# Kernel tuning notes

Measured on AMD Instinct MI355X. Metric: run time of the kernel, lower is better.

Reference implementation:

```python
import jax, jax.numpy as jnp
import numpy as np

TOKENS, IN_DIM, HID, OUT_DIM = 32768, 256, 1024, 256
N_EXP, TOP_K = 8, 2


def setup_inputs() -> dict:
    key = jax.random.key(0)
    ks = jax.random.split(key, 6)
    s_in = 1.0 / np.sqrt(IN_DIM)
    s_hid = 1.0 / np.sqrt(HID)
    return {
        "x": jax.random.normal(ks[0], (TOKENS, IN_DIM), dtype=jnp.float32),
        "Wg": jax.random.uniform(ks[1], (IN_DIM, N_EXP), jnp.float32, -s_in, s_in),
        "W1": jax.random.uniform(ks[2], (N_EXP, IN_DIM, HID), jnp.float32, -s_in, s_in),
        "b1": jax.random.uniform(ks[3], (N_EXP, HID), jnp.float32, -s_in, s_in),
        "W2": jax.random.uniform(ks[4], (N_EXP, HID, OUT_DIM), jnp.float32, -s_hid, s_hid),
        "b2": jax.random.uniform(ks[5], (N_EXP, OUT_DIM), jnp.float32, -s_hid, s_hid),
    }


def reference(x, Wg, W1, b1, W2, b2):
    # Router: softmax over expert logits, pick top-k, renormalize weights
    logits = x @ Wg                                  # [B, E]
    router_probs = jax.nn.softmax(logits, axis=-1)   # [B, E]
    top_w, top_idx = jax.lax.top_k(router_probs, TOP_K)  # [B, K]
    top_w = top_w / jnp.sum(top_w, axis=-1, keepdims=True)
    # Dense all-expert compute (faithful to the torch.stack over experts)
    h = jax.nn.relu(jnp.einsum("bi,eih->beh", x, W1) + b1[None])   # [B, E, H]
    expert_out = jnp.einsum("beh,eho->beo", h, W2) + b2[None]       # [B, E, O]
    # Gather top-k experts per token and combine
    selected = jnp.take_along_axis(expert_out, top_idx[:, :, None], axis=1)  # [B, K, O]
    output = jnp.sum(selected * top_w[:, :, None], axis=1)                   # [B, O]
    return output, router_probs
```

## Files before the change

kernel.cpp:

```cpp
#include <hip/hip_runtime.h>
#include <hip/hip_bf16.h>
#include <stdint.h>

#define T_TOK 32768
#define IN_D  256
#define HID_D 1024
#define OUT_D 256
#define NE    8
#define BM    64
#define HC    32
#define NCH   (HID_D / HC)

typedef unsigned short u16;
typedef __attribute__((ext_vector_type(8))) __bf16 bf16x8;
typedef __attribute__((ext_vector_type(4))) float f32x4;
typedef __attribute__((ext_vector_type(4))) unsigned int u32x4;
typedef __attribute__((ext_vector_type(2))) unsigned int u32x2;

__device__ __forceinline__ u16 f2bf(float f) {
  unsigned int u = __builtin_bit_cast(unsigned int, f);
  u = (u + 0x7FFFu + ((u >> 16) & 1u)) >> 16;
  return (u16)u;
}

__device__ __forceinline__ void gload_lds16(const u16* g, u16* l) {
  __builtin_amdgcn_global_load_lds(
      (const __attribute__((address_space(1))) unsigned int*)g,
      (__attribute__((address_space(3))) unsigned int*)l, 16, 0, 0);
}

__global__ __launch_bounds__(64) void pack_w1_kernel(const float* __restrict__ W1,
                                                     u16* __restrict__ w1p) {
  int b = blockIdx.x;
  int f = b & 15, c = (b >> 4) & 31, e = b >> 9;
  int l = threadIdx.x, l15 = l & 15, l4 = l >> 4;
  int h = c * 32 + (f >> 3) * 16 + l15;
  int k0 = (f & 7) * 32 + l4 * 8;
  unsigned int w[4];
#pragma unroll
  for (int p = 0; p < 4; ++p) {
    u16 a = f2bf(W1[((size_t)e * IN_D + k0 + 2 * p) * HID_D + h]);
    u16 bq = f2bf(W1[((size_t)e * IN_D + k0 + 2 * p + 1) * HID_D + h]);
    w[p] = (unsigned int)a | ((unsigned int)bq << 16);
  }
  *reinterpret_cast<u32x4*>(w1p + (size_t)b * 512 + l * 8) = u32x4{w[0], w[1], w[2], w[3]};
}

__global__ __launch_bounds__(64) void pack_w2_kernel(const float* __restrict__ W2,
                                                     u16* __restrict__ w2p) {
  int b = blockIdx.x;
  int f = b & 15, c = (b >> 4) & 31, e = b >> 9;
  int l = threadIdx.x, l15 = l & 15, l4 = l >> 4;
  int o = f * 16 + l15;
  int k0 = c * 32 + l4 * 8;
  unsigned int w[4];
#pragma unroll
  for (int p = 0; p < 4; ++p) {
    u16 a = f2bf(W2[((size_t)e * HID_D + k0 + 2 * p) * OUT_D + o]);
    u16 bq = f2bf(W2[((size_t)e * HID_D + k0 + 2 * p + 1) * OUT_D + o]);
    w[p] = (unsigned int)a | ((unsigned int)bq << 16);
  }
  *reinterpret_cast<u32x4*>(w2p + (size_t)b * 512 + l * 8) = u32x4{w[0], w[1], w[2], w[3]};
}

__global__ __launch_bounds__(256) void router_kernel(
    const float* __restrict__ x, const float* __restrict__ Wg,
    u16* __restrict__ xbf, float* __restrict__ probs, int* __restrict__ counts,
    int* __restrict__ list_tok, float* __restrict__ list_w) {
  __shared__ float wg_s[IN_D * NE];
  __shared__ int lcnt[NE];
  __shared__ int gbase[NE];
  int tid = threadIdx.x;
  for (int i = tid; i < IN_D * NE; i += 256) wg_s[i] = Wg[i];
  if (tid < NE) lcnt[tid] = 0;
  __syncthreads();

  int lane = tid & 63;
  int wave = tid >> 6;
  int q = lane & 3;
  int tk = blockIdx.x * 64 + wave * 16 + (lane >> 2);

  float acc[NE];
#pragma unroll
  for (int e = 0; e < NE; ++e) acc[e] = 0.f;
  const float* xrow = x + (size_t)tk * IN_D;
  u16* xbrow = xbf + (size_t)tk * IN_D;
#pragma unroll
  for (int i = 0; i < 16; ++i) {
    int c = i * 4 + q;
    f32x4 v = *reinterpret_cast<const f32x4*>(xrow + c * 4);
    unsigned int lo = (unsigned int)f2bf(v[0]) | ((unsigned int)f2bf(v[1]) << 16);
    unsigned int hi = (unsigned int)f2bf(v[2]) | ((unsigned int)f2bf(v[3]) << 16);
    *reinterpret_cast<u32x2*>(xbrow + c * 4) = u32x2{lo, hi};
#pragma unroll
    for (int j = 0; j < 4; ++j) {
      const float* wr = &wg_s[(c * 4 + j) * NE];
#pragma unroll
      for (int e = 0; e < NE; ++e) acc[e] = fmaf(v[j], wr[e], acc[e]);
    }
  }
#pragma unroll
  for (int e = 0; e < NE; ++e) {
    acc[e] += __shfl_xor(acc[e], 1);
    acc[e] += __shfl_xor(acc[e], 2);
  }
  float m = acc[0];
#pragma unroll
  for (int e = 1; e < NE; ++e) m = fmaxf(m, acc[e]);
  float p[NE], s = 0.f;
#pragma unroll
  for (int e = 0; e < NE; ++e) { p[e] = expf(acc[e] - m); s += p[e]; }
  float inv = 1.f / s;
#pragma unroll
  for (int e = 0; e < NE; ++e) p[e] *= inv;
  int i0 = 0; float p0 = p[0];
#pragma unroll
  for (int e = 1; e < NE; ++e) if (p[e] > p0) { p0 = p[e]; i0 = e; }
  int i1 = -1; float p1 = -1.f;
#pragma unroll
  for (int e = 0; e < NE; ++e) if (e != i0 && p[e] > p1) { p1 = p[e]; i1 = e; }
  float wsum = p0 + p1;

  int lp0 = 0, lp1 = 0;
  if (q == 0) {
    *reinterpret_cast<f32x4*>(probs + (size_t)tk * NE)     = f32x4{p[0], p[1], p[2], p[3]};
    *reinterpret_cast<f32x4*>(probs + (size_t)tk * NE + 4) = f32x4{p[4], p[5], p[6], p[7]};
    lp0 = atomicAdd(&lcnt[i0], 1);
    lp1 = atomicAdd(&lcnt[i1], 1);
  }
  __syncthreads();
  if (tid < NE) gbase[tid] = atomicAdd(&counts[tid], lcnt[tid]);
  __syncthreads();
  if (q == 0) {
    int e0 = gbase[i0] + lp0;
    list_tok[(size_t)i0 * T_TOK + e0] = tk;
    list_w[(size_t)i0 * T_TOK + e0] = p0 / wsum;
    int e1 = gbase[i1] + lp1;
    list_tok[(size_t)i1 * T_TOK + e1] = tk | (1 << 16);
    list_w[(size_t)i1 * T_TOK + e1] = p1 / wsum;
  }
}

__global__ __launch_bounds__(512, 4) void moe_main_kernel(
    const u16* __restrict__ xbf, const u16* __restrict__ w1p,
    const u16* __restrict__ w2p, const float* __restrict__ b1,
    const float* __restrict__ b2, const int* __restrict__ counts,
    const int* __restrict__ list_tok, const float* __restrict__ list_w,
    float* __restrict__ part) {
  int e = blockIdx.x & 7;
  int tile = blockIdx.x >> 3;
  int cnt = counts[e];
  int base = tile * BM;
  if (base >= cnt) return;

  __shared__ __align__(16) u16 W1s[2][16 * 512];
  __shared__ __align__(16) u16 W2s[2][16 * 512];
  __shared__ __align__(16) u16 Hs[4 * 512];
  __shared__ float Bs[HID_D];
  __shared__ int toks[BM];
  __shared__ float gw[BM];

  int tid = threadIdx.x;
  int wave = tid >> 6;
  int lane = tid & 63;
  const int l15 = lane & 15;
  const int l4 = lane >> 4;
  const int hh = wave & 1;
  const int tt = wave >> 1;

  if (tid < BM) {
    int idx = base + tid;
    int tv = 0; float w = 0.f;
    if (idx < cnt) { tv = list_tok[(size_t)e * T_TOK + idx]; w = list_w[(size_t)e * T_TOK + idx]; }
    toks[tid] = tv;
    gw[tid] = w;
  }
#pragma unroll
  for (int j = 0; j < 2; ++j) Bs[tid + j * 512] = b1[(size_t)e * HID_D + tid + j * 512];

  const u16* w1base = w1p + (size_t)e * NCH * 16 * 512;
  const u16* w2base = w2p + (size_t)e * NCH * 16 * 512;

  auto stage = [&](int c, int buf) {
#pragma unroll
    for (int j2 = 0; j2 < 4; ++j2) {
      int f = wave * 4 + j2;
      if (f < 16)
        gload_lds16(w1base + ((size_t)c * 16 + f) * 512 + lane * 8, &W1s[buf][f * 512]);
      else
        gload_lds16(w2base + ((size_t)c * 16 + (f - 16)) * 512 + lane * 8,
                    &W2s[buf][(f - 16) * 512]);
    }
  };

  stage(0, 0);
  __syncthreads();

  u32x4 bx[8];
  {
    const u16* xr = xbf + (size_t)(toks[tt * 16 + l15] & 0xFFFF) * IN_D + l4 * 8;
#pragma unroll
    for (int kk = 0; kk < 8; ++kk)
      bx[kk] = __builtin_nontemporal_load(reinterpret_cast<const u32x4*>(xr + kk * 32));
  }

  f32x4 acc[2][4];
#pragma unroll
  for (int a = 0; a < 2; ++a)
#pragma unroll
    for (int b = 0; b < 4; ++b) acc[a][b] = f32x4{0.f, 0.f, 0.f, 0.f};

#pragma unroll 1
  for (int c = 0; c < NCH; ++c) {
    int buf = c & 1;
    if (c + 1 < NCH) stage(c + 1, buf ^ 1);

    {
      f32x4 accH = f32x4{0.f, 0.f, 0.f, 0.f};
#pragma unroll
      for (int kk = 0; kk < 8; ++kk) {
        const char* pa = reinterpret_cast<const char*>(&W1s[buf][0]) +
                         (hh * 8 + kk) * 1024 + lane * 16;
        bf16x8 a = __builtin_bit_cast(bf16x8, *reinterpret_cast<const u32x4*>(pa));
        accH = __builtin_amdgcn_mfma_f32_16x16x32_bf16(a, __builtin_bit_cast(bf16x8, bx[kk]), accH, 0, 0, 0);
      }
      f32x4 bias = *reinterpret_cast<const f32x4*>(&Bs[c * HC + hh * 16 + l4 * 4]);
      u16 q0 = f2bf(fmaxf(accH[0] + bias[0], 0.f));
      u16 q1 = f2bf(fmaxf(accH[1] + bias[1], 0.f));
      u16 q2 = f2bf(fmaxf(accH[2] + bias[2], 0.f));
      u16 q3 = f2bf(fmaxf(accH[3] + bias[3], 0.f));
      unsigned int lo = (unsigned int)q0 | ((unsigned int)q1 << 16);
      unsigned int hi = (unsigned int)q2 | ((unsigned int)q3 << 16);
      char* p = reinterpret_cast<char*>(&Hs[0]) + tt * 1024 +
                ((hh * 2 + (l4 >> 1)) * 16 + l15) * 16 + (l4 & 1) * 8;
      *reinterpret_cast<u32x2*>(p) = u32x2{lo, hi};
    }
    asm volatile("s_waitcnt lgkmcnt(0)" ::: "memory");
    __builtin_amdgcn_s_barrier();

    {
#pragma unroll
      for (int of = 0; of < 2; ++of) {
        const char* pa = reinterpret_cast<const char*>(&W2s[buf][0]) +
                         (wave * 2 + of) * 1024 + lane * 16;
        bf16x8 a = __builtin_bit_cast(bf16x8, *reinterpret_cast<const u32x4*>(pa));
#pragma unroll
        for (int tf = 0; tf < 4; ++tf) {
          bf16x8 bh = __builtin_bit_cast(bf16x8, *reinterpret_cast<const u32x4*>(
              reinterpret_cast<const char*>(&Hs[0]) + tf * 1024 + lane * 16));
          acc[of][tf] = __builtin_amdgcn_mfma_f32_16x16x32_bf16(a, bh, acc[of][tf], 0, 0, 0);
        }
      }
    }
    asm volatile("s_waitcnt vmcnt(0)" ::: "memory");
    __builtin_amdgcn_s_barrier();
  }

#pragma unroll
  for (int of = 0; of < 2; ++of) {
    int ob = (wave * 2 + of) * 16 + l4 * 4;
    f32x4 bv = *reinterpret_cast<const f32x4*>(b2 + (size_t)e * OUT_D + ob);
#pragma unroll
    for (int tf = 0; tf < 4; ++tf) {
      int trow = tf * 16 + l15;
      if (base + trow < cnt) {
        int tv = toks[trow];
        int tok = tv & 0xFFFF;
        int slot = tv >> 16;
        float w = gw[trow];
        f32x4 o;
#pragma unroll
        for (int r = 0; r < 4; ++r) o[r] = w * (acc[of][tf][r] + bv[r]);
        __builtin_nontemporal_store(
            o, reinterpret_cast<f32x4*>(part + ((size_t)slot * T_TOK + tok) * OUT_D + ob));
      }
    }
  }
}

__global__ __launch_bounds__(256) void combine_kernel(const float* __restrict__ part,
                                                      float* __restrict__ out) {
  size_t i = (size_t)blockIdx.x * 256 + threadIdx.x;
  f32x4 a = __builtin_nontemporal_load(reinterpret_cast<const f32x4*>(part) + i);
  f32x4 b = __builtin_nontemporal_load(
      reinterpret_cast<const f32x4*>(part + (size_t)T_TOK * OUT_D) + i);
  f32x4 o = a + b;
  __builtin_nontemporal_store(o, reinterpret_cast<f32x4*>(out) + i);
}

extern "C" void kernel_launch(void* const* d_in, const int* in_sizes, int n_in,
                              void* d_out, int out_size, void* d_ws, size_t ws_size,
                              hipStream_t stream) {
  const float* x  = (const float*)d_in[0];
  const float* Wg = (const float*)d_in[1];
  const float* W1 = (const float*)d_in[2];
  const float* b1 = (const float*)d_in[3];
  const float* W2 = (const float*)d_in[4];
  const float* b2 = (const float*)d_in[5];
  float* out = (float*)d_out;

  char* ws = (char*)d_ws;
  constexpr size_t OFF_XBF  = 0;
  constexpr size_t OFF_W1P  = (size_t)T_TOK * IN_D * 2;
  constexpr size_t OFF_W2P  = OFF_W1P + (size_t)NE * HID_D * IN_D * 2;
  constexpr size_t OFF_CNT  = OFF_W2P + (size_t)NE * OUT_D * HID_D * 2;
  constexpr size_t OFF_LTOK = OFF_CNT + 128;
  constexpr size_t OFF_LW   = OFF_LTOK + (size_t)NE * T_TOK * 4;
  constexpr size_t OFF_PART = OFF_LW + (size_t)NE * T_TOK * 4;

  u16*   xbf      = (u16*)(ws + OFF_XBF);
  u16*   w1p      = (u16*)(ws + OFF_W1P);
  u16*   w2p      = (u16*)(ws + OFF_W2P);
  int*   counts   = (int*)(ws + OFF_CNT);
  int*   list_tok = (int*)(ws + OFF_LTOK);
  float* list_w   = (float*)(ws + OFF_LW);
  float* part     = (float*)(ws + OFF_PART);
  float* probs    = out + (size_t)T_TOK * OUT_D;

  hipMemsetAsync(counts, 0, NE * sizeof(int), stream);

  pack_w1_kernel<<<NE * NCH * 16, 64, 0, stream>>>(W1, w1p);
  pack_w2_kernel<<<NE * NCH * 16, 64, 0, stream>>>(W2, w2p);
  router_kernel<<<T_TOK / 64, 256, 0, stream>>>(x, Wg, xbf, probs, counts,
                                                list_tok, list_w);

  moe_main_kernel<<<(T_TOK / BM) * NE, 512, 0, stream>>>(
      xbf, w1p, w2p, b1, b2, counts, list_tok, list_w, part);

  combine_kernel<<<(T_TOK * OUT_D / 4) / 256, 256, 0, stream>>>(part, out);
}
```

Baseline: 160.1 us.

## Software-pipeline expert MLP chunks with W2 in registers and double-buffered hidden tile

Each wave now loads its W2 fragment for a chunk straight from global memory into registers instead of staging it through LDS. The hidden tile is double-buffered, so the second GEMM of chunk c runs in the same barrier phase as the first GEMM of chunk c+1. This cuts the loop from two barriers per chunk to one and shrinks the LDS footprint. The trade-off is more register pressure from the W2 prefetch buffers, plus direct global loads whose latency must hide behind the MFMA work.

```diff
diff --git a/kernel.cpp b/kernel.cpp
--- a/kernel.cpp
+++ b/kernel.cpp
@@ -154,8 +154,7 @@
   if (base >= cnt) return;
 
   __shared__ __align__(16) u16 W1s[2][16 * 512];
-  __shared__ __align__(16) u16 W2s[2][16 * 512];
-  __shared__ __align__(16) u16 Hs[4 * 512];
+  __shared__ __align__(16) u16 Hs[2][4 * 512];
   __shared__ float Bs[HID_D];
   __shared__ int toks[BM];
   __shared__ float gw[BM];
@@ -183,14 +182,16 @@
 
   auto stage = [&](int c, int buf) {
 #pragma unroll
-    for (int j2 = 0; j2 < 4; ++j2) {
-      int f = wave * 4 + j2;
-      if (f < 16)
-        gload_lds16(w1base + ((size_t)c * 16 + f) * 512 + lane * 8, &W1s[buf][f * 512]);
-      else
-        gload_lds16(w2base + ((size_t)c * 16 + (f - 16)) * 512 + lane * 8,
-                    &W2s[buf][(f - 16) * 512]);
-    }
+    for (int j2 = 0; j2 < 2; ++j2) {
+      int f = wave * 2 + j2;
+      gload_lds16(w1base + ((size_t)c * 16 + f) * 512 + lane * 8, &W1s[buf][f * 512]);
+    }
+  };
+  auto loadW2 = [&](int c, u32x4* w2r) {
+#pragma unroll
+    for (int of = 0; of < 2; ++of)
+      w2r[of] = *reinterpret_cast<const u32x4*>(
+          w2base + ((size_t)c * 16 + wave * 2 + of) * 512 + lane * 8);
   };
 
   stage(0, 0);
@@ -204,57 +205,74 @@
       bx[kk] = __builtin_nontemporal_load(reinterpret_cast<const u32x4*>(xr + kk * 32));
   }
 
+  u32x4 w2A[2], w2B[2];
   f32x4 acc[2][4];
 #pragma unroll
   for (int a = 0; a < 2; ++a)
 #pragma unroll
     for (int b = 0; b < 4; ++b) acc[a][b] = f32x4{0.f, 0.f, 0.f, 0.f};
 
+  auto p1 = [&](int c, int wb, int hb) {
+    f32x4 accH = f32x4{0.f, 0.f, 0.f, 0.f};
+#pragma unroll
+    for (int kk = 0; kk < 8; ++kk) {
+      const char* pa = reinterpret_cast<const char*>(&W1s[wb][0]) +
+                       (hh * 8 + kk) * 1024 + lane * 16;
+      bf16x8 a = __builtin_bit_cast(bf16x8, *reinterpret_cast<const u32x4*>(pa));
+      accH = __builtin_amdgcn_mfma_f32_16x16x32_bf16(a, __builtin_bit_cast(bf16x8, bx[kk]), accH, 0, 0, 0);
+    }
+    f32x4 bias = *reinterpret_cast<const f32x4*>(&Bs[c * HC + hh * 16 + l4 * 4]);
+    u16 q0 = f2bf(fmaxf(accH[0] + bias[0], 0.f));
+    u16 q1 = f2bf(fmaxf(accH[1] + bias[1], 0.f));
+    u16 q2 = f2bf(fmaxf(accH[2] + bias[2], 0.f));
+    u16 q3 = f2bf(fmaxf(accH[3] + bias[3], 0.f));
+    unsigned int lo = (unsigned int)q0 | ((unsigned int)q1 << 16);
+    unsigned int hi = (unsigned int)q2 | ((unsigned int)q3 << 16);
+    char* p = reinterpret_cast<char*>(&Hs[hb][0]) + tt * 1024 +
+              ((hh * 2 + (l4 >> 1)) * 16 + l15) * 16 + (l4 & 1) * 8;
+    *reinterpret_cast<u32x2*>(p) = u32x2{lo, hi};
+  };
+
+  auto p2 = [&](int hb, const u32x4* w2r) {
+    bf16x8 bh[4];
+#pragma unroll
+    for (int tf = 0; tf < 4; ++tf)
+      bh[tf] = __builtin_bit_cast(bf16x8, *reinterpret_cast<const u32x4*>(
+          reinterpret_cast<const char*>(&Hs[hb][0]) + tf * 1024 + lane * 16));
+#pragma unroll
+    for (int of = 0; of < 2; ++of) {
+      bf16x8 a = __builtin_bit_cast(bf16x8, w2r[of]);
+#pragma unroll
+      for (int tf = 0; tf < 4; ++tf)
+        acc[of][tf] = __builtin_amdgcn_mfma_f32_16x16x32_bf16(a, bh[tf], acc[of][tf], 0, 0, 0);
+    }
+  };
+
+  loadW2(0, w2A);
+  p1(0, 0, 0);
+  stage(1, 1);
+  loadW2(1, w2B);
+  asm volatile("s_waitcnt vmcnt(0) lgkmcnt(0)" ::: "memory");
+  __builtin_amdgcn_s_barrier();
+
 #pragma unroll 1
-  for (int c = 0; c < NCH; ++c) {
-    int buf = c & 1;
-    if (c + 1 < NCH) stage(c + 1, buf ^ 1);
-
-    {
-      f32x4 accH = f32x4{0.f, 0.f, 0.f, 0.f};
-#pragma unroll
-      for (int kk = 0; kk < 8; ++kk) {
-        const char* pa = reinterpret_cast<const char*>(&W1s[buf][0]) +
-                         (hh * 8 + kk) * 1024 + lane * 16;
-        bf16x8 a = __builtin_bit_cast(bf16x8, *reinterpret_cast<const u32x4*>(pa));
-        accH = __builtin_amdgcn_mfma_f32_16x16x32_bf16(a, __builtin_bit_cast(bf16x8, bx[kk]), accH, 0, 0, 0);
-      }
-      f32x4 bias = *reinterpret_cast<const f32x4*>(&Bs[c * HC + hh * 16 + l4 * 4]);
-      u16 q0 = f2bf(fmaxf(accH[0] + bias[0], 0.f));
-      u16 q1 = f2bf(fmaxf(accH[1] + bias[1], 0.f));
-      u16 q2 = f2bf(fmaxf(accH[2] + bias[2], 0.f));
-      u16 q3 = f2bf(fmaxf(accH[3] + bias[3], 0.f));
-      unsigned int lo = (unsigned int)q0 | ((unsigned int)q1 << 16);
-      unsigned int hi = (unsigned int)q2 | ((unsigned int)q3 << 16);
-      char* p = reinterpret_cast<char*>(&Hs[0]) + tt * 1024 +
-                ((hh * 2 + (l4 >> 1)) * 16 + l15) * 16 + (l4 & 1) * 8;
-      *reinterpret_cast<u32x2*>(p) = u32x2{lo, hi};
-    }
-    asm volatile("s_waitcnt lgkmcnt(0)" ::: "memory");
+  for (int c = 1; c < NCH; c += 2) {
+    if (c + 1 < NCH) stage(c + 1, 0);
+    p2(0, w2A);
+    if (c + 1 < NCH) loadW2(c + 1, w2A);
+    p1(c, 1, 1);
+    asm volatile("s_waitcnt vmcnt(0) lgkmcnt(0)" ::: "memory");
     __builtin_amdgcn_s_barrier();
-
-    {
-#pragma unroll
-      for (int of = 0; of < 2; ++of) {
-        const char* pa = reinterpret_cast<const char*>(&W2s[buf][0]) +
-                         (wave * 2 + of) * 1024 + lane * 16;
-        bf16x8 a = __builtin_bit_cast(bf16x8, *reinterpret_cast<const u32x4*>(pa));
-#pragma unroll
-        for (int tf = 0; tf < 4; ++tf) {
-          bf16x8 bh = __builtin_bit_cast(bf16x8, *reinterpret_cast<const u32x4*>(
-              reinterpret_cast<const char*>(&Hs[0]) + tf * 1024 + lane * 16));
-          acc[of][tf] = __builtin_amdgcn_mfma_f32_16x16x32_bf16(a, bh, acc[of][tf], 0, 0, 0);
-        }
-      }
-    }
-    asm volatile("s_waitcnt vmcnt(0)" ::: "memory");
-    __builtin_amdgcn_s_barrier();
-  }
+    if (c + 1 < NCH) {
+      if (c + 2 < NCH) stage(c + 2, 1);
+      p2(1, w2B);
+      if (c + 2 < NCH) loadW2(c + 2, w2B);
+      p1(c + 1, 0, 0);
+      asm volatile("s_waitcnt vmcnt(0) lgkmcnt(0)" ::: "memory");
+      __builtin_amdgcn_s_barrier();
+    }
+  }
+  p2(1, w2B);
 
 #pragma unroll
   for (int of = 0; of < 2; ++of) {
```

Result: no change. 161.3 us (median of 2 runs) (+0.7%).
